# Performance work log

Measured on AMD Instinct MI355X. Metric: run time of the kernel, lower is better.

Reference implementation:

```python
import jax, jax.numpy as jnp
import numpy as np

N, C, E = 100000, 128, 1600000


def setup_inputs() -> dict:
    key = jax.random.key(0)
    ks = jax.random.split(key, 7)
    s = 1.0 / np.sqrt(C)
    return {
        "x": jax.random.normal(ks[0], (N, C), jnp.float32),
        "edge_index": jax.random.randint(ks[1], (2, E), 0, N),
        "weight": jax.random.uniform(ks[2], (C, C), jnp.float32, -s, s),   # GCN weight (evolved)
        "w_ih": jax.random.uniform(ks[3], (4 * C, C), jnp.float32, -s, s),  # LSTM input weights
        "w_hh": jax.random.uniform(ks[4], (4 * C, C), jnp.float32, -s, s),  # LSTM hidden weights (h0=0 -> no fwd effect)
        "b_ih": jax.random.uniform(ks[5], (4 * C,), jnp.float32, -s, s),
        "b_hh": jax.random.uniform(ks[6], (4 * C,), jnp.float32, -s, s),
    }


def reference(x, edge_index, weight, w_ih, w_hh, b_ih, b_hh):
    n = x.shape[0]
    # --- LSTM single step over the weight matrix (seq=1, batch=C, h0=c0=0) ---
    # h0 = 0 so w_hh contributes nothing to the forward pass.
    gates = weight @ w_ih.T + b_ih + b_hh  # [C, 4C]
    i, f, g, o = jnp.split(gates, 4, axis=1)
    c = jax.nn.sigmoid(i) * jnp.tanh(g)           # f-gate * c0 = 0
    w_new = jax.nn.sigmoid(o) * jnp.tanh(c)       # evolved GCN weight [C, C]
    del w_hh  # zero forward contribution, kept for faithfulness

    xw = x @ w_new  # [N, C]
    loop = jnp.arange(n)
    src = jnp.concatenate([edge_index[0], loop])  # source j
    dst = jnp.concatenate([edge_index[1], loop])  # target i
    ew = jnp.ones(src.shape[0], x.dtype)          # edge_weight defaults to 1 (improved=False -> self-loop weight 1)
    deg = jax.ops.segment_sum(ew, dst, num_segments=n)
    dinv = jnp.where(deg > 0, jax.lax.rsqrt(jnp.maximum(deg, 1e-12)), 0.0)
    norm = dinv[src] * dinv[dst]                  # [E+N]
    # gather messages, scale, scatter-add to targets
    return jax.ops.segment_sum(xw[src] * norm[:, None], dst, num_segments=n)
```

## Files before the change

### kernel.cpp

```cpp
#include <hip/hip_runtime.h>
#include <hip/hip_bf16.h>
#include <math.h>

typedef __hip_bfloat16  bf16_t;
typedef __attribute__((ext_vector_type(8))) short  short8;
typedef __attribute__((ext_vector_type(4))) float  f32x4;
typedef __attribute__((ext_vector_type(4))) int    intv4;

#define CDIM 128
#define KCAP 32

static __device__ __forceinline__ float sigm(float x){ return 1.0f/(1.0f+__expf(-x)); }
static __device__ __forceinline__ float bflo(unsigned u){ return __builtin_bit_cast(float, u << 16); }
static __device__ __forceinline__ float bfhi(unsigned u){ return __builtin_bit_cast(float, u & 0xffff0000u); }
static __device__ __forceinline__ unsigned short f2bf_u(float f){
    __hip_bfloat16 h = __float2bfloat16(f);
    return __builtin_bit_cast(unsigned short, h);
}
static __device__ __forceinline__ unsigned packbf(float a, float b){
    return (unsigned)f2bf_u(a) | ((unsigned)f2bf_u(b) << 16);
}
static __device__ __forceinline__ short f2bf_s(float f){
    return (short)f2bf_u(f);
}

__global__ void k_lstm(const float* __restrict__ weight, const float* __restrict__ w_ih,
                       const float* __restrict__ b_ih,   const float* __restrict__ b_hh,
                       short* __restrict__ wfrag, int* __restrict__ zptr, int zcount){
    const int gtid = blockIdx.x*CDIM + threadIdx.x;
    for(int i = gtid; i < zcount; i += CDIM*CDIM) zptr[i] = 0;

    __shared__ float wrow[CDIM];
    const int r = blockIdx.x, j = threadIdx.x;
    wrow[j] = weight[r*CDIM + j];
    __syncthreads();
    const float4* wi = (const float4*)(w_ih + (size_t)j*CDIM);
    const float4* wg = (const float4*)(w_ih + (size_t)(2*CDIM + j)*CDIM);
    const float4* wo = (const float4*)(w_ih + (size_t)(3*CDIM + j)*CDIM);
    const float4* wr = (const float4*)wrow;
    float si = 0.f, sg = 0.f, so = 0.f;
    #pragma unroll 8
    for(int k = 0; k < CDIM/4; k++){
        float4 w4 = wr[k];
        float4 a = wi[k]; si += w4.x*a.x + w4.y*a.y + w4.z*a.z + w4.w*a.w;
        float4 b = wg[k]; sg += w4.x*b.x + w4.y*b.y + w4.z*b.z + w4.w*b.w;
        float4 c = wo[k]; so += w4.x*c.x + w4.y*c.y + w4.z*c.z + w4.w*c.w;
    }
    si += b_ih[j]        + b_hh[j];
    sg += b_ih[2*CDIM+j] + b_hh[2*CDIM+j];
    so += b_ih[3*CDIM+j] + b_hh[3*CDIM+j];
    float c  = sigm(si)*tanhf(sg);
    float wv = sigm(so)*tanhf(c);
    const int t = r >> 5, quad = (r >> 3) & 3, jj = r & 7;
    const int n0 = j >> 4, mm = j & 15;
    wfrag[((size_t)((t*8 + n0)*64 + quad*16 + mm))*8 + jj] = f2bf_s(wv);
}

__global__ __launch_bounds__(256) void k_fillfix(const int* __restrict__ src, const int* __restrict__ dst,
        int e, int* __restrict__ cnt, int* __restrict__ csr,
        int2* __restrict__ spill, int* __restrict__ spillc, int nper){
    const int grp  = blockIdx.x & 7;
    const int lo   = grp*nper, hi = lo + nper;
    const int t4   = (blockIdx.x >> 3)*256 + threadIdx.x;
    const int step = (gridDim.x >> 3)*256;
    if((e & 3) == 0){
        const int e4 = e >> 2;
        const intv4* d4 = (const intv4*)dst;
        const intv4* s4 = (const intv4*)src;
        for(int i = t4; i < e4; i += step){
            intv4 d = __builtin_nontemporal_load(d4 + i);
            intv4 s = __builtin_nontemporal_load(s4 + i);
            #pragma unroll
            for(int c = 0; c < 4; c++){
                int di = d[c];
                if(di >= lo && di < hi){
                    int p = atomicAdd(&cnt[di], 1);
                    if(p < KCAP) csr[(size_t)di*KCAP + p] = s[c];
                    else { int sp = atomicAdd(spillc, 1); spill[sp] = make_int2(s[c], di); }
                }
            }
        }
    } else {
        for(int i = t4; i < e; i += step){
            int di = __builtin_nontemporal_load(dst + i);
            if(di >= lo && di < hi){
                int sv = __builtin_nontemporal_load(src + i);
                int p = atomicAdd(&cnt[di], 1);
                if(p < KCAP) csr[(size_t)di*KCAP + p] = sv;
                else { int sp = atomicAdd(spillc, 1); spill[sp] = make_int2(sv, di); }
            }
        }
    }
}

__global__ __launch_bounds__(256) void k_offscale(const float* __restrict__ x,
        const int* __restrict__ deg, bf16_t* __restrict__ y, int n){
    __shared__ float sdinv[256];
    const int base = blockIdx.x*256;
    const int t = threadIdx.x;
    const int i = base + t;
    float dv = 0.f;
    if(i < n) dv = rsqrtf((float)(deg[i] + 1));
    sdinv[t] = dv;
    __syncthreads();
    const int wid = t >> 6, lane = t & 63;
    for(int r = wid; r < 256; r += 4){
        int row = base + r;
        if(row >= n) break;
        float di = sdinv[r];
        float2 v = ((const float2*)(x + (size_t)row*CDIM))[lane];
        ((unsigned*)(y + (size_t)row*CDIM))[lane] = packbf(di*v.x, di*v.y);
    }
}

__global__ __launch_bounds__(256) void k_agg(const bf16_t* __restrict__ y, const int* __restrict__ csr,
                      const int* __restrict__ deg, const int2* __restrict__ spill,
                      const int* __restrict__ spillc, bf16_t* __restrict__ agg, int n){
    const int node = (int)(((size_t)blockIdx.x*256 + threadIdx.x) >> 6);
    if(node >= n) return;
    const int lane = threadIdx.x & 63;
    const int q = lane >> 4, f = lane & 15;
    const int   cnt = deg[node];
    const float di  = rsqrtf((float)(cnt + 1));
    const int   m   = cnt < KCAP ? cnt : KCAP;
    const uint4* yrow = (const uint4*)y;
    uint4 sv = yrow[(size_t)node*16 + f];
    int jid = (lane < m) ? csr[(size_t)node*KCAP + lane] : 0;

    int jv[8];
    #pragma unroll
    for(int t = 0; t < 8; t++) jv[t] = __shfl(jid, 4*t + q, 64);

    uint4 v[8];
    #pragma unroll
    for(int t = 0; t < 8; t++)
        if(4*t + q < m) v[t] = yrow[(size_t)jv[t]*16 + f];

    float acc[8];
    #pragma unroll
    for(int i = 0; i < 8; i++) acc[i] = 0.f;
    #pragma unroll
    for(int t = 0; t < 8; t++){
        if(4*t + q < m){
            acc[0] += bflo(v[t].x); acc[1] += bfhi(v[t].x);
            acc[2] += bflo(v[t].y); acc[3] += bfhi(v[t].y);
            acc[4] += bflo(v[t].z); acc[5] += bfhi(v[t].z);
            acc[6] += bflo(v[t].w); acc[7] += bfhi(v[t].w);
        }
    }
    int sc = *spillc;
    if(sc > 0){
        for(int t = q; t < sc; t += 4){
            int2 sd = spill[t];
            if(sd.y == node){
                uint4 vv = yrow[(size_t)sd.x*16 + f];
                acc[0] += bflo(vv.x); acc[1] += bfhi(vv.x);
                acc[2] += bflo(vv.y); acc[3] += bfhi(vv.y);
                acc[4] += bflo(vv.z); acc[5] += bfhi(vv.z);
                acc[6] += bflo(vv.w); acc[7] += bfhi(vv.w);
            }
        }
    }
    #pragma unroll
    for(int i = 0; i < 8; i++){
        acc[i] += __shfl_xor(acc[i], 16, 64);
        acc[i] += __shfl_xor(acc[i], 32, 64);
    }
    if(q == 0){
        uint4 o;
        o.x = packbf(di*(acc[0] + bflo(sv.x)), di*(acc[1] + bfhi(sv.x)));
        o.y = packbf(di*(acc[2] + bflo(sv.y)), di*(acc[3] + bfhi(sv.y)));
        o.z = packbf(di*(acc[4] + bflo(sv.z)), di*(acc[5] + bfhi(sv.z)));
        o.w = packbf(di*(acc[6] + bflo(sv.w)), di*(acc[7] + bfhi(sv.w)));
        ((uint4*)agg)[(size_t)node*16 + f] = o;
    }
}

__global__ __launch_bounds__(256) void k_mgemm(const bf16_t* __restrict__ agg,
                                               const short* __restrict__ wfrag,
                                               float* __restrict__ out, int n){
    const int wid  = blockIdx.x*4 + (threadIdx.x >> 6);
    const int row0 = wid*16;
    if(row0 >= n) return;
    const int lane = threadIdx.x & 63;
    const int m    = lane & 15, quad = lane >> 4;
    int arow = row0 + m; if(arow > n-1) arow = n-1;
    const short* ap = (const short*)agg + (size_t)arow*CDIM + quad*8;
    short8 a0 = *(const short8*)(ap);
    short8 a1 = *(const short8*)(ap + 32);
    short8 a2 = *(const short8*)(ap + 64);
    short8 a3 = *(const short8*)(ap + 96);
    const short8* bp = (const short8*)wfrag;
    float* orow = out + (size_t)(row0 + quad*4)*CDIM + m;
    const bool full = (row0 + 16 <= n);
    #pragma unroll
    for(int n0 = 0; n0 < 8; n0++){
        f32x4 acc = {0.f, 0.f, 0.f, 0.f};
        acc = __builtin_amdgcn_mfma_f32_16x16x32_bf16(a0, bp[(0*8+n0)*64 + lane], acc, 0, 0, 0);
        acc = __builtin_amdgcn_mfma_f32_16x16x32_bf16(a1, bp[(1*8+n0)*64 + lane], acc, 0, 0, 0);
        acc = __builtin_amdgcn_mfma_f32_16x16x32_bf16(a2, bp[(2*8+n0)*64 + lane], acc, 0, 0, 0);
        acc = __builtin_amdgcn_mfma_f32_16x16x32_bf16(a3, bp[(3*8+n0)*64 + lane], acc, 0, 0, 0);
        if(full){
            #pragma unroll
            for(int r = 0; r < 4; r++)
                orow[(size_t)r*CDIM + n0*16] = acc[r];
        } else {
            #pragma unroll
            for(int r = 0; r < 4; r++)
                if(row0 + quad*4 + r < n) orow[(size_t)r*CDIM + n0*16] = acc[r];
        }
    }
}

extern "C" void kernel_launch(void* const* d_in, const int* in_sizes, int n_in,
                              void* d_out, int out_size, void* d_ws, size_t ws_size,
                              hipStream_t stream){
    const float* x      = (const float*)d_in[0];
    const int*   ei     = (const int*)  d_in[1];
    const float* weight = (const float*)d_in[2];
    const float* w_ih   = (const float*)d_in[3];
    const float* b_ih   = (const float*)d_in[5];
    const float* b_hh   = (const float*)d_in[6];
    float* out = (float*)d_out;

    const int n = in_sizes[0]/CDIM;
    const int e = in_sizes[1]/2;
    const int* srcp = ei;
    const int* dstp = ei + e;

    auto alignup = [](size_t v){ return (v + 255) & ~(size_t)255; };
    char*  base = (char*)d_ws;
    size_t o = 0;
    short*  wfrag  = (short*) (base+o); o += alignup((size_t)CDIM*CDIM*sizeof(short));
    int*    deg    = (int*)   (base+o); o += alignup((size_t)n*4);
    int*    spillc = (int*)   (base+o); o += alignup(256);
    size_t  zbytes = (size_t)((char*)(base+o) - (char*)deg);
    int*    csr    = (int*)   (base+o); o += alignup((size_t)n*KCAP*4);
    bf16_t* aggbuf = (bf16_t*)(base+o);

    bf16_t* y     = (bf16_t*)d_out;
    int2*   spill = (int2*)((char*)d_out + (size_t)n*CDIM*sizeof(bf16_t));

    const int nper = (n + 7)/8;
    const int pb = 2048;
    const int nb = (n + 255)/256;
    const int rb = (n + 3)/4;
    const int gw = (n + 15)/16;
    const int gb = (gw + 3)/4;

    k_lstm    <<<CDIM, CDIM, 0, stream>>>(weight, w_ih, b_ih, b_hh, wfrag,
                                          deg, (int)(zbytes/4));
    k_fillfix <<<pb, 256, 0, stream>>>(srcp, dstp, e, deg, csr, spill, spillc, nper);
    k_offscale<<<nb, 256, 0, stream>>>(x, deg, y, n);
    k_agg     <<<rb, 256, 0, stream>>>(y, csr, deg, spill, spillc, aggbuf, n);
    k_mgemm   <<<gb, 256, 0, stream>>>(aggbuf, wfrag, out, n);
}
```

Before: 316.6 us.

## Fuse x-to-bf16 cast into CSR fill kernel and apply source norm in aggregation

Removes the separate offscale kernel, which needed the finished degree counts, by doing an unscaled bf16 cast of x inside extra blocks of the CSR-fill launch so the cast overlaps the edge pass. The source-side D^-1/2 factor is now applied in the aggregation kernel, which gathers deg[j] per neighbor and computes rsqrt on the fly. This drops one launch and the serialization between degree counting and scaling, at the cost of extra random degree loads in aggregation and fewer blocks for the edge pass.

Measured after the change: 277.2 us (median of 2 runs). -12.4%, faster.

```diff
diff --git a/kernel.cpp b/kernel.cpp
--- a/kernel.cpp
+++ b/kernel.cpp
@@ -56,60 +56,52 @@
     wfrag[((size_t)((t*8 + n0)*64 + quad*16 + mm))*8 + jj] = f2bf_s(wv);
 }
 
-__global__ __launch_bounds__(256) void k_fillfix(const int* __restrict__ src, const int* __restrict__ dst,
+__global__ __launch_bounds__(256) void k_fillcast(const int* __restrict__ src, const int* __restrict__ dst,
         int e, int* __restrict__ cnt, int* __restrict__ csr,
-        int2* __restrict__ spill, int* __restrict__ spillc, int nper){
-    const int grp  = blockIdx.x & 7;
-    const int lo   = grp*nper, hi = lo + nper;
-    const int t4   = (blockIdx.x >> 3)*256 + threadIdx.x;
-    const int step = (gridDim.x >> 3)*256;
-    if((e & 3) == 0){
-        const int e4 = e >> 2;
-        const intv4* d4 = (const intv4*)dst;
-        const intv4* s4 = (const intv4*)src;
-        for(int i = t4; i < e4; i += step){
-            intv4 d = __builtin_nontemporal_load(d4 + i);
-            intv4 s = __builtin_nontemporal_load(s4 + i);
-            #pragma unroll
-            for(int c = 0; c < 4; c++){
-                int di = d[c];
-                if(di >= lo && di < hi){
-                    int p = atomicAdd(&cnt[di], 1);
-                    if(p < KCAP) csr[(size_t)di*KCAP + p] = s[c];
-                    else { int sp = atomicAdd(spillc, 1); spill[sp] = make_int2(s[c], di); }
-                }
+        int2* __restrict__ spill, int* __restrict__ spillc, int nper,
+        const float* __restrict__ x, bf16_t* __restrict__ y0, int nf4,
+        int castblocks, int edgeblocks){
+    if((int)blockIdx.x < castblocks){
+        const float4* xv = (const float4*)x;
+        uint2* yv = (uint2*)y0;
+        const int t0   = blockIdx.x*256 + threadIdx.x;
+        const int step = castblocks*256;
+        for(int i = t0; i < nf4; i += step){
+            float4 v = xv[i];
+            uint2 o; o.x = packbf(v.x, v.y); o.y = packbf(v.z, v.w);
+            yv[i] = o;
+        }
+        return;
+    }
+    const int bid = (int)blockIdx.x - castblocks;
+    const int grp = bid & 7;
+    const int lo  = grp*nper, hi = lo + nper;
+    const int tid = (bid >> 3)*256 + threadIdx.x;
+    const int nt  = (edgeblocks >> 3)*256;
+    const int e4  = e >> 2;
+    const intv4* d4 = (const intv4*)dst;
+    const intv4* s4 = (const intv4*)src;
+    for(int i = tid; i < e4; i += nt){
+        intv4 d = __builtin_nontemporal_load(d4 + i);
+        intv4 s = __builtin_nontemporal_load(s4 + i);
+        #pragma unroll
+        for(int c = 0; c < 4; c++){
+            int di = d[c];
+            if(di >= lo && di < hi){
+                int p = atomicAdd(&cnt[di], 1);
+                if(p < KCAP) csr[(size_t)di*KCAP + p] = s[c];
+                else { int sp = atomicAdd(spillc, 1); spill[sp] = make_int2(s[c], di); }
             }
         }
-    } else {
-        for(int i = t4; i < e; i += step){
-            int di = __builtin_nontemporal_load(dst + i);
-            if(di >= lo && di < hi){
-                int sv = __builtin_nontemporal_load(src + i);
-                int p = atomicAdd(&cnt[di], 1);
-                if(p < KCAP) csr[(size_t)di*KCAP + p] = sv;
-                else { int sp = atomicAdd(spillc, 1); spill[sp] = make_int2(sv, di); }
-            }
-        }
-    }
-}
-
-__global__ __launch_bounds__(256) void k_offscale(const float* __restrict__ x,
-        const int* __restrict__ deg, bf16_t* __restrict__ y, int n){
-    __shared__ float sdinv[256];
-    const int base = blockIdx.x*256;
-    const int t = threadIdx.x;
-    const int i = base + t;
-    float dv = 0.f;
-    if(i < n) dv = rsqrtf((float)(deg[i] + 1));
-    sdinv[t] = dv;
-    __syncthreads();
-    const int wid = t >> 6, lane = t & 63;
-    for(int r = wid; r < 256; r += 4){
-        int row = base + r;
-        if(row >= n) break;
-        float di = sdinv[r];
-        float2 v = ((const float2*)(x + (size_t)row*CDIM))[lane];
-        ((unsigned*)(y + (size_t)row*CDIM))[lane] = packbf(di*v.x, di*v.y);
+    }
+    for(int k = e4*4 + tid; k < e; k += nt){
+        int di = dst[k];
+        if(di >= lo && di < hi){
+            int sv = src[k];
+            int p = atomicAdd(&cnt[di], 1);
+            if(p < KCAP) csr[(size_t)di*KCAP + p] = sv;
+            else { int sp = atomicAdd(spillc, 1); spill[sp] = make_int2(sv, di); }
+        }
     }
 }
 
@@ -131,6 +123,11 @@
     #pragma unroll
     for(int t = 0; t < 8; t++) jv[t] = __shfl(jid, 4*t + q, 64);
 
+    int dgv[8];
+    #pragma unroll
+    for(int t = 0; t < 8; t++)
+        if(4*t + q < m) dgv[t] = deg[jv[t]];
+
     uint4 v[8];
     #pragma unroll
     for(int t = 0; t < 8; t++)
@@ -142,10 +139,11 @@
     #pragma unroll
     for(int t = 0; t < 8; t++){
         if(4*t + q < m){
-            acc[0] += bflo(v[t].x); acc[1] += bfhi(v[t].x);
-            acc[2] += bflo(v[t].y); acc[3] += bfhi(v[t].y);
-            acc[4] += bflo(v[t].z); acc[5] += bfhi(v[t].z);
-            acc[6] += bflo(v[t].w); acc[7] += bfhi(v[t].w);
+            float dj = rsqrtf((float)(dgv[t] + 1));
+            acc[0] += dj*bflo(v[t].x); acc[1] += dj*bfhi(v[t].x);
+            acc[2] += dj*bflo(v[t].y); acc[3] += dj*bfhi(v[t].y);
+            acc[4] += dj*bflo(v[t].z); acc[5] += dj*bfhi(v[t].z);
+            acc[6] += dj*bflo(v[t].w); acc[7] += dj*bfhi(v[t].w);
         }
     }
     int sc = *spillc;
@@ -153,11 +151,12 @@
         for(int t = q; t < sc; t += 4){
             int2 sd = spill[t];
             if(sd.y == node){
+                float dj = rsqrtf((float)(deg[sd.x] + 1));
                 uint4 vv = yrow[(size_t)sd.x*16 + f];
-                acc[0] += bflo(vv.x); acc[1] += bfhi(vv.x);
-                acc[2] += bflo(vv.y); acc[3] += bfhi(vv.y);
-                acc[4] += bflo(vv.z); acc[5] += bfhi(vv.z);
-                acc[6] += bflo(vv.w); acc[7] += bfhi(vv.w);
+                acc[0] += dj*bflo(vv.x); acc[1] += dj*bfhi(vv.x);
+                acc[2] += dj*bflo(vv.y); acc[3] += dj*bfhi(vv.y);
+                acc[4] += dj*bflo(vv.z); acc[5] += dj*bfhi(vv.z);
+                acc[6] += dj*bflo(vv.w); acc[7] += dj*bfhi(vv.w);
             }
         }
     }
@@ -168,10 +167,10 @@
     }
     if(q == 0){
         uint4 o;
-        o.x = packbf(di*(acc[0] + bflo(sv.x)), di*(acc[1] + bfhi(sv.x)));
-        o.y = packbf(di*(acc[2] + bflo(sv.y)), di*(acc[3] + bfhi(sv.y)));
-        o.z = packbf(di*(acc[4] + bflo(sv.z)), di*(acc[5] + bfhi(sv.z)));
-        o.w = packbf(di*(acc[6] + bflo(sv.w)), di*(acc[7] + bfhi(sv.w)));
+        o.x = packbf(di*(acc[0] + di*bflo(sv.x)), di*(acc[1] + di*bfhi(sv.x)));
+        o.y = packbf(di*(acc[2] + di*bflo(sv.y)), di*(acc[3] + di*bfhi(sv.y)));
+        o.z = packbf(di*(acc[4] + di*bflo(sv.z)), di*(acc[5] + di*bfhi(sv.z)));
+        o.w = packbf(di*(acc[6] + di*bflo(sv.w)), di*(acc[7] + di*bfhi(sv.w)));
         ((uint4*)agg)[(size_t)node*16 + f] = o;
     }
 }
@@ -238,20 +237,20 @@
     int*    csr    = (int*)   (base+o); o += alignup((size_t)n*KCAP*4);
     bf16_t* aggbuf = (bf16_t*)(base+o);
 
-    bf16_t* y     = (bf16_t*)d_out;
+    bf16_t* y0    = (bf16_t*)d_out;
     int2*   spill = (int2*)((char*)d_out + (size_t)n*CDIM*sizeof(bf16_t));
 
-    const int nper = (n + 7)/8;
-    const int pb = 2048;
-    const int nb = (n + 255)/256;
+    const int nper  = (n + 7)/8;
+    const int castb = 512;
+    const int edgeb = 1536;
     const int rb = (n + 3)/4;
     const int gw = (n + 15)/16;
     const int gb = (gw + 3)/4;
 
     k_lstm    <<<CDIM, CDIM, 0, stream>>>(weight, w_ih, b_ih, b_hh, wfrag,
                                           deg, (int)(zbytes/4));
-    k_fillfix <<<pb, 256, 0, stream>>>(srcp, dstp, e, deg, csr, spill, spillc, nper);
-    k_offscale<<<nb, 256, 0, stream>>>(x, deg, y, n);
-    k_agg     <<<rb, 256, 0, stream>>>(y, csr, deg, spill, spillc, aggbuf, n);
+    k_fillcast<<<castb+edgeb, 256, 0, stream>>>(srcp, dstp, e, deg, csr, spill, spillc, nper,
+                                                x, y0, n*CDIM/4, castb, edgeb);
+    k_agg     <<<rb, 256, 0, stream>>>(y0, csr, deg, spill, spillc, aggbuf, n);
     k_mgemm   <<<gb, 256, 0, stream>>>(aggbuf, wfrag, out, n);
 }
```
